# Kernel optimization log

Measured on AMD Instinct MI355X. Metric: run time of the kernel, lower is better.

## Reference

```python
import jax, jax.numpy as jnp
import numpy as np

B = 65536      # batch
DIM = 32       # flow dimension
NH = 24        # hidden width of each per-dim MLP
PARITY = False # order = reversed(range(dim)) when parity is False
NEG_SLOPE = 0.2


def _causal_mask(dim, dtype):
    # mask[k, j] = 1 if j <= k ; stacked layer k corresponds to torch layer i=k+1
    # which sees x[:, :i] = columns 0..k
    return (jnp.arange(dim)[None, :] <= jnp.arange(dim - 1)[:, None]).astype(dtype)


def setup_inputs() -> dict:
    key = jax.random.key(0)
    ks = jax.random.split(key, 10)
    s = 0.1
    x = jax.random.normal(ks[0], (B, DIM), jnp.float32)
    p0 = jax.random.normal(ks[1], (2,), jnp.float32) * s          # LeafParam(2)
    W1 = jax.random.normal(ks[2], (DIM - 1, NH, DIM), jnp.float32) * s
    W1 = W1 * _causal_mask(DIM, jnp.float32)[:, None, :]          # zero padded cols j > k
    b1 = jax.random.normal(ks[3], (DIM - 1, NH), jnp.float32) * s
    W2 = jax.random.normal(ks[4], (DIM - 1, NH, NH), jnp.float32) * s
    b2 = jax.random.normal(ks[5], (DIM - 1, NH), jnp.float32) * s
    W3 = jax.random.normal(ks[6], (DIM - 1, NH, NH), jnp.float32) * s
    b3 = jax.random.normal(ks[7], (DIM - 1, NH), jnp.float32) * s
    W4 = jax.random.normal(ks[8], (DIM - 1, 2, NH), jnp.float32) * s
    b4 = jax.random.normal(ks[9], (DIM - 1, 2), jnp.float32) * s
    return {"x": x, "p0": p0, "W1": W1, "b1": b1, "W2": W2, "b2": b2,
            "W3": W3, "b3": b3, "W4": W4, "b4": b4}


def reference(x, p0, W1, b1, W2, b2, W3, b3, W4, b4):
    # SlowMAF.forward: per-dim MLP(x[:, :i]) -> (s, t); z[:, order[i]] = x[:, i]*exp(s)+t
    # All dim-1 tiny MLPs are fused into stacked batched GEMMs; the growing slice
    # x[:, :i] is realized via a causal mask on the first-layer weights (same math).
    Bsz, dim = x.shape
    lrelu = lambda h: jnp.where(h > 0, h, NEG_SLOPE * h)  # LeakyReLU(0.2)
    W1m = W1 * _causal_mask(dim, x.dtype)[:, None, :]
    h = lrelu(jnp.einsum('bd,khd->bkh', x, W1m) + b1)      # (B, dim-1, NH)
    h = lrelu(jnp.einsum('bkh,kHh->bkH', h, W2) + b2)
    h = lrelu(jnp.einsum('bkh,kHh->bkH', h, W3) + b3)
    st = jnp.einsum('bkh,koh->bko', h, W4) + b4            # (B, dim-1, 2)
    st0 = jnp.broadcast_to(p0[None, None, :], (Bsz, 1, 2)) # LeafParam for dim 0
    st_all = jnp.concatenate([st0, st], axis=1)            # (B, dim, 2)
    s = st_all[..., 0]
    t = st_all[..., 1]
    vals = x * jnp.exp(s) + t                              # (B, dim)
    order = jnp.arange(dim) if PARITY else jnp.arange(dim)[::-1]
    z = jnp.zeros_like(x).at[:, order].set(vals)
    log_det = jnp.sum(s, axis=1)                           # (B,)
    return z, log_det
```

## Files before the change

### kernel.cpp

```cpp
#include <hip/hip_runtime.h>

#define BATCH 65536
#define DIM 32

typedef short    sfrag8 __attribute__((ext_vector_type(8)));
typedef _Float16 hfrag8 __attribute__((ext_vector_type(8)));
typedef _Float16 h2     __attribute__((ext_vector_type(2)));
typedef float    f32x16 __attribute__((ext_vector_type(16)));
typedef unsigned u32x4  __attribute__((ext_vector_type(4)));

__device__ __forceinline__ short f2h(float v) {
    _Float16 h = (_Float16)v;
    return __builtin_bit_cast(short, h);
}

__device__ __forceinline__ h2 cvt2h(float a, float b) {
    return __builtin_bit_cast(h2, __builtin_amdgcn_cvt_pkrtz(a, b));
}

__device__ __forceinline__ unsigned pack2h(float a, float b) {
    return __builtin_bit_cast(unsigned, __builtin_amdgcn_cvt_pkrtz(a, b));
}

__device__ float frag_elem(int k, int f, int r, int h, int j,
    const float* W1, const float* b1, const float* W2, const float* b2,
    const float* W3, const float* b3, const float* W4, const float* b4)
{
    if (f == 0) return (r < 24) ? W1[k*768 + r*32 + 8*h + j] : 0.f;
    if (f == 1) {
        if (r >= 24) return 0.f;
        int c = 16 + 8*h + j;
        if (c == 31) return b1[k*24 + r];
        return W1[k*768 + r*32 + c];
    }
    const float* W; const float* bb; int R;
    if (f < 4)      { W = W2 + k*576; bb = b2 + k*24; R = 24; }
    else if (f < 6) { W = W3 + k*576; bb = b3 + k*24; R = 24; }
    else            { W = W4 + k*48;  bb = b4 + k*2;  R = 2;  }
    if (r >= R) return 0.f;
    if ((f & 1) == 0) {
        int feat = j + 4*h + (j >= 4 ? 4 : 0);
        return W[r*24 + feat];
    } else {
        if (j < 4)            return W[r*24 + 16 + 4*h + j];
        if (j == 4 && h == 0) return bb[r];
        return 0.f;
    }
}

__global__ __launch_bounds__(256) void prep_frags(
    const float* __restrict__ W1, const float* __restrict__ b1,
    const float* __restrict__ W2, const float* __restrict__ b2,
    const float* __restrict__ W3, const float* __restrict__ b3,
    const float* __restrict__ W4, const float* __restrict__ b4,
    short* __restrict__ wsf)
{
    int t = blockIdx.x * 256 + threadIdx.x;
    int lane = t & 63, f = (t >> 6) & 7, k = t >> 9;
    int r = lane & 31, h = lane >> 5;
    sfrag8 o;
    #pragma unroll
    for (int j = 0; j < 8; j++)
        o[j] = f2h(frag_elem(k, f, r, h, j, W1, b1, W2, b2, W3, b3, W4, b4));
    *(sfrag8*)(wsf + (size_t)t * 8) = o;
}

__device__ __forceinline__ void transition(const f32x16 a, unsigned c1,
                                           hfrag8& blo, hfrag8& bhi)
{
    const h2 s02 = {(_Float16)0.2f, (_Float16)0.2f};
    unsigned P[6];
    #pragma unroll
    for (int g = 0; g < 6; g++) {
        h2 v = cvt2h(a[2*g], a[2*g + 1]);
        h2 rr = __builtin_elementwise_max(v, v * s02);
        P[g] = __builtin_bit_cast(unsigned, rr);
    }
    blo = __builtin_bit_cast(hfrag8, (u32x4){P[0], P[1], P[2], P[3]});
    bhi = __builtin_bit_cast(hfrag8, (u32x4){P[4], P[5], c1, 0u});
}

template<bool PREPPED>
__global__ __launch_bounds__(256, 4) void maf2(
    const float* __restrict__ x, const float* __restrict__ p0,
    const float* __restrict__ W1, const float* __restrict__ b1,
    const float* __restrict__ W2, const float* __restrict__ b2,
    const float* __restrict__ W3, const float* __restrict__ b3,
    const float* __restrict__ W4, const float* __restrict__ b4,
    const short* __restrict__ wsf,
    float* __restrict__ out)
{
    __shared__ float4 lds[2048];

    const int  kg   = blockIdx.y;
    const int  lane = threadIdx.x & 63;
    const int  wave = threadIdx.x >> 6;
    const bool hi   = lane >= 32;
    const int  h    = hi ? 1 : 0;
    const int  r    = lane & 31;
    const int  k0   = kg ? 4*kg - 1 : 0;
    const int  nk   = kg ? 4 : 3;
    const int  c0   = 28 - 4*kg;
    const int  colbase = (blockIdx.x * 4 + wave) * 64;
    const unsigned c1 = hi ? 0u : 0x3C00u;

    hfrag8 xlo[2], xhi[2];
    float  xa[2][4];

    if constexpr (PREPPED) {
        const float4* xg = (const float4*)(x + (size_t)blockIdx.x * 256 * DIM);
        #pragma unroll
        for (int j = 0; j < 8; j++) {
            int a16 = j * 256 + threadIdx.x;
            int c = a16 >> 3, q = a16 & 7;
            lds[c*8 + (q ^ (c & 7))] = xg[a16];
        }
        __syncthreads();

        #pragma unroll
        for (int t = 0; t < 2; t++) {
            int c = wave*64 + t*32 + r;
            int s = c & 7;
            float4 q0 = lds[c*8 + ((2*h)     ^ s)];
            float4 q1 = lds[c*8 + ((2*h + 1) ^ s)];
            float4 q2 = lds[c*8 + ((4 + 2*h) ^ s)];
            float4 q3 = lds[c*8 + ((5 + 2*h) ^ s)];
            float4 qa = lds[c*8 + (kg ^ s)];
            unsigned L0 = pack2h(q0.x, q0.y), L1 = pack2h(q0.z, q0.w);
            unsigned L2 = pack2h(q1.x, q1.y), L3 = pack2h(q1.z, q1.w);
            unsigned H0 = pack2h(q2.x, q2.y), H1 = pack2h(q2.z, q2.w);
            unsigned H2 = pack2h(q3.x, q3.y);
            unsigned H3 = pack2h(q3.z, hi ? 1.0f : q3.w);
            xlo[t] = __builtin_bit_cast(hfrag8, (u32x4){L0, L1, L2, L3});
            xhi[t] = __builtin_bit_cast(hfrag8, (u32x4){H0, H1, H2, H3});
            xa[t][0] = qa.x; xa[t][1] = qa.y; xa[t][2] = qa.z; xa[t][3] = qa.w;
        }
        __syncthreads();

        {
            const float4* src = (const float4*)(wsf + (size_t)k0 * 4096);
            #pragma unroll
            for (int c = 0; c < 8; c++) {
                int u = c * 256 + threadIdx.x;
                lds[u] = src[u];
            }
        }
        __syncthreads();
    } else {
        #pragma unroll
        for (int t = 0; t < 2; t++) {
            const float* xp = x + (size_t)(colbase + t*32 + r) * DIM;
            float4 q0 = *(const float4*)(xp + 8*h);
            float4 q1 = *(const float4*)(xp + 8*h + 4);
            float4 q2 = *(const float4*)(xp + 16 + 8*h);
            float4 q3 = *(const float4*)(xp + 16 + 8*h + 4);
            unsigned L0 = pack2h(q0.x, q0.y), L1 = pack2h(q0.z, q0.w);
            unsigned L2 = pack2h(q1.x, q1.y), L3 = pack2h(q1.z, q1.w);
            unsigned H0 = pack2h(q2.x, q2.y), H1 = pack2h(q2.z, q2.w);
            unsigned H2 = pack2h(q3.x, q3.y);
            unsigned H3 = pack2h(q3.z, hi ? 1.0f : q3.w);
            xlo[t] = __builtin_bit_cast(hfrag8, (u32x4){L0, L1, L2, L3});
            xhi[t] = __builtin_bit_cast(hfrag8, (u32x4){H0, H1, H2, H3});
            float4 qa = *(const float4*)(xp + 4*kg);
            xa[t][0] = qa.x; xa[t][1] = qa.y; xa[t][2] = qa.z; xa[t][3] = qa.w;
        }
    }

    f32x16 Z;
    #pragma unroll
    for (int q = 0; q < 16; q++) Z[q] = 0.f;

    float za[2][4];
    float ld[2] = {0.f, 0.f};

    const _Float16* lds_f = (const _Float16*)lds;

    #pragma unroll
    for (int i = 0; i < 4; i++) {
        if (i < nk) {
            hfrag8 Fa, Fb;
            if constexpr (PREPPED) {
                const _Float16* lf = lds_f + i * 4096;
                #define LDF(ff) (*(const hfrag8*)(lf + (ff)*512 + lane*8))

                Fa = LDF(0); Fb = LDF(1);
                f32x16 aA = __builtin_amdgcn_mfma_f32_32x32x16_f16(Fa, xlo[0], Z, 0, 0, 0);
                f32x16 aB = __builtin_amdgcn_mfma_f32_32x32x16_f16(Fa, xlo[1], Z, 0, 0, 0);
                aA = __builtin_amdgcn_mfma_f32_32x32x16_f16(Fb, xhi[0], aA, 0, 0, 0);
                aB = __builtin_amdgcn_mfma_f32_32x32x16_f16(Fb, xhi[1], aB, 0, 0, 0);
                Fa = LDF(2); Fb = LDF(3);
                hfrag8 loA, hA, loB, hB;
                transition(aA, c1, loA, hA);
                transition(aB, c1, loB, hB);
                aA = __builtin_amdgcn_mfma_f32_32x32x16_f16(Fa, loA, Z, 0, 0, 0);
                aB = __builtin_amdgcn_mfma_f32_32x32x16_f16(Fa, loB, Z, 0, 0, 0);
                aA = __builtin_amdgcn_mfma_f32_32x32x16_f16(Fb, hA, aA, 0, 0, 0);
                aB = __builtin_amdgcn_mfma_f32_32x32x16_f16(Fb, hB, aB, 0, 0, 0);
                Fa = LDF(4); Fb = LDF(5);
                transition(aA, c1, loA, hA);
                transition(aB, c1, loB, hB);
                aA = __builtin_amdgcn_mfma_f32_32x32x16_f16(Fa, loA, Z, 0, 0, 0);
                aB = __builtin_amdgcn_mfma_f32_32x32x16_f16(Fa, loB, Z, 0, 0, 0);
                aA = __builtin_amdgcn_mfma_f32_32x32x16_f16(Fb, hA, aA, 0, 0, 0);
                aB = __builtin_amdgcn_mfma_f32_32x32x16_f16(Fb, hB, aB, 0, 0, 0);
                Fa = LDF(6); Fb = LDF(7);
                transition(aA, c1, loA, hA);
                transition(aB, c1, loB, hB);
                aA = __builtin_amdgcn_mfma_f32_32x32x16_f16(Fa, loA, Z, 0, 0, 0);
                aB = __builtin_amdgcn_mfma_f32_32x32x16_f16(Fa, loB, Z, 0, 0, 0);
                aA = __builtin_amdgcn_mfma_f32_32x32x16_f16(Fb, hA, aA, 0, 0, 0);
                aB = __builtin_amdgcn_mfma_f32_32x32x16_f16(Fb, hB, aB, 0, 0, 0);
                #undef LDF

                float sA = aA[0], tA = aA[1];
                float sB = aB[0], tB = aB[1];
                float eA = __expf(sA), eB = __expf(sB);
                if (kg) {
                    za[0][3 - i] = xa[0][i] * eA + tA;
                    za[1][3 - i] = xa[1][i] * eB + tB;
                } else if (i < 3) {
                    za[0][2 - i] = xa[0][i + 1] * eA + tA;
                    za[1][2 - i] = xa[1][i + 1] * eB + tB;
                }
                ld[0] += sA; ld[1] += sB;
            } else {
                int k = k0 + i;
                hfrag8 F[8];
                #pragma unroll
                for (int f = 0; f < 8; f++)
                    #pragma unroll
                    for (int j = 0; j < 8; j++)
                        F[f][j] = (_Float16)frag_elem(k, f, r, h, j,
                                                      W1, b1, W2, b2, W3, b3, W4, b4);
                #pragma unroll
                for (int t = 0; t < 2; t++) {
                    f32x16 a1  = __builtin_amdgcn_mfma_f32_32x32x16_f16(F[0], xlo[t], Z, 0, 0, 0);
                    f32x16 acc = __builtin_amdgcn_mfma_f32_32x32x16_f16(F[1], xhi[t], a1, 0, 0, 0);
                    hfrag8 blo, bh2;
                    transition(acc, c1, blo, bh2);
                    a1  = __builtin_amdgcn_mfma_f32_32x32x16_f16(F[2], blo, Z, 0, 0, 0);
                    acc = __builtin_amdgcn_mfma_f32_32x32x16_f16(F[3], bh2, a1, 0, 0, 0);
                    transition(acc, c1, blo, bh2);
                    a1  = __builtin_amdgcn_mfma_f32_32x32x16_f16(F[4], blo, Z, 0, 0, 0);
                    acc = __builtin_amdgcn_mfma_f32_32x32x16_f16(F[5], bh2, a1, 0, 0, 0);
                    transition(acc, c1, blo, bh2);
                    a1  = __builtin_amdgcn_mfma_f32_32x32x16_f16(F[6], blo, Z, 0, 0, 0);
                    acc = __builtin_amdgcn_mfma_f32_32x32x16_f16(F[7], bh2, a1, 0, 0, 0);
                    float sv = acc[0], tv = acc[1];
                    float e  = __expf(sv);
                    if (kg) { za[t][3 - i] = xa[t][i] * e + tv; }
                    else if (i < 3) { za[t][2 - i] = xa[t][i + 1] * e + tv; }
                    ld[t] += sv;
                }
            }
        }
    }

    if (kg == 0) {
        float s0 = p0[0], t0 = p0[1];
        float e0 = __expf(s0);
        #pragma unroll
        for (int t = 0; t < 2; t++) {
            za[t][3] = xa[t][0] * e0 + t0;
            ld[t] += s0;
        }
    }

    if (!hi) {
        #pragma unroll
        for (int t = 0; t < 2; t++) {
            int b = colbase + t*32 + r;
            float4 v; v.x = za[t][0]; v.y = za[t][1]; v.z = za[t][2]; v.w = za[t][3];
            *(float4*)(out + (size_t)b * DIM + c0) = v;
            atomicAdd(out + (size_t)BATCH * DIM + b, ld[t]);
        }
    }
}

extern "C" void kernel_launch(void* const* d_in, const int* in_sizes, int n_in,
                              void* d_out, int out_size, void* d_ws, size_t ws_size,
                              hipStream_t stream)
{
    const float* x  = (const float*)d_in[0];
    const float* p0 = (const float*)d_in[1];
    const float* W1 = (const float*)d_in[2];
    const float* b1 = (const float*)d_in[3];
    const float* W2 = (const float*)d_in[4];
    const float* b2 = (const float*)d_in[5];
    const float* W3 = (const float*)d_in[6];
    const float* b3 = (const float*)d_in[7];
    const float* W4 = (const float*)d_in[8];
    const float* b4 = (const float*)d_in[9];
    float* out = (float*)d_out;

    const size_t FRG = (size_t)31 * 8 * 64 * 8;
    if (ws_size >= FRG * sizeof(short)) {
        short* wsf = (short*)d_ws;
        prep_frags<<<62, 256, 0, stream>>>(W1, b1, W2, b2, W3, b3, W4, b4, wsf);
        maf2<true><<<dim3(256, 8), 256, 0, stream>>>(
            x, p0, W1, b1, W2, b2, W3, b3, W4, b4, wsf, out);
    } else {
        maf2<false><<<dim3(256, 8), 256, 0, stream>>>(
            x, p0, W1, b1, W2, b2, W3, b3, W4, b4, nullptr, out);
    }
}
```

Measured before the change: 95.03 us.

## Write per-group partials to workspace and reduce with a separate transpose kernel

Instead of each k-group block writing strided float4 pieces into the output rows and atomically adding log-det, the main kernel now writes contiguous per-group partial z and log-det arrays to workspace. A new reduce kernel gathers the 8 groups per batch row, reassembles each row through swizzled shared memory for coalesced output writes, and sums log-det without atomics. This removes atomics and the scattered 16-byte stores but adds an extra kernel launch and a round trip through workspace memory, and it needs a larger workspace.

```diff
diff --git a/kernel.cpp b/kernel.cpp
--- a/kernel.cpp
+++ b/kernel.cpp
@@ -88,6 +88,7 @@
     const float* __restrict__ W3, const float* __restrict__ b3,
     const float* __restrict__ W4, const float* __restrict__ b4,
     const short* __restrict__ wsf,
+    float* __restrict__ zpart, float* __restrict__ ldpart,
     float* __restrict__ out)
 {
     __shared__ float4 lds[2048];
@@ -271,10 +272,45 @@
         for (int t = 0; t < 2; t++) {
             int b = colbase + t*32 + r;
             float4 v; v.x = za[t][0]; v.y = za[t][1]; v.z = za[t][2]; v.w = za[t][3];
-            *(float4*)(out + (size_t)b * DIM + c0) = v;
-            atomicAdd(out + (size_t)BATCH * DIM + b, ld[t]);
-        }
-    }
+            if constexpr (PREPPED) {
+                *(float4*)(zpart + ((size_t)kg * BATCH + b) * 4) = v;
+                ldpart[(size_t)kg * BATCH + b] = ld[t];
+            } else {
+                *(float4*)(out + (size_t)b * DIM + c0) = v;
+                atomicAdd(out + (size_t)BATCH * DIM + b, ld[t]);
+            }
+        }
+    }
+}
+
+__global__ __launch_bounds__(256) void reduce_z(
+    const float* __restrict__ zpart, const float* __restrict__ ldpart,
+    float* __restrict__ out)
+{
+    __shared__ float4 lds[2048];
+    const int tid = threadIdx.x;
+    const int col = blockIdx.x * 256 + tid;
+
+    float4 rq[8];
+    float ldsum = 0.f;
+    #pragma unroll
+    for (int g = 0; g < 8; g++) {
+        rq[7 - g] = *(const float4*)(zpart + ((size_t)g * BATCH + col) * 4);
+        ldsum += ldpart[(size_t)g * BATCH + col];
+    }
+    #pragma unroll
+    for (int q = 0; q < 8; q++)
+        lds[tid*8 + (q ^ (tid & 7))] = rq[q];
+    __syncthreads();
+
+    float4* og = (float4*)out + (size_t)blockIdx.x * 2048;
+    #pragma unroll
+    for (int j = 0; j < 8; j++) {
+        int a16 = j * 256 + tid;
+        int c = a16 >> 3, q = a16 & 7;
+        og[a16] = lds[c*8 + (q ^ (c & 7))];
+    }
+    out[(size_t)BATCH * DIM + col] = ldsum;
 }
 
 extern "C" void kernel_launch(void* const* d_in, const int* in_sizes, int n_in,
@@ -293,14 +329,20 @@
     const float* b4 = (const float*)d_in[9];
     float* out = (float*)d_out;
 
-    const size_t FRG = (size_t)31 * 8 * 64 * 8;
-    if (ws_size >= FRG * sizeof(short)) {
-        short* wsf = (short*)d_ws;
+    const size_t ZP_OFF = (size_t)16 << 20;
+    const size_t LD_OFF = (size_t)28 << 20;
+    const size_t NEED   = (size_t)30 << 20;
+
+    if (ws_size >= NEED) {
+        short* wsf   = (short*)d_ws;
+        float* zpart = (float*)((char*)d_ws + ZP_OFF);
+        float* ldpart= (float*)((char*)d_ws + LD_OFF);
         prep_frags<<<62, 256, 0, stream>>>(W1, b1, W2, b2, W3, b3, W4, b4, wsf);
         maf2<true><<<dim3(256, 8), 256, 0, stream>>>(
-            x, p0, W1, b1, W2, b2, W3, b3, W4, b4, wsf, out);
+            x, p0, W1, b1, W2, b2, W3, b3, W4, b4, wsf, zpart, ldpart, out);
+        reduce_z<<<256, 256, 0, stream>>>(zpart, ldpart, out);
     } else {
         maf2<false><<<dim3(256, 8), 256, 0, stream>>>(
-            x, p0, W1, b1, W2, b2, W3, b3, W4, b4, nullptr, out);
-    }
-}
+            x, p0, W1, b1, W2, b2, W3, b3, W4, b4, nullptr, nullptr, nullptr, out);
+    }
+}
```

Result: slower. 99.13 us (+4.3%).
